# Optimization experiments

Measured on AMD Instinct MI355X. Metric: run time of the kernel, lower is better.

## Reference

```python
import jax, jax.numpy as jnp
import numpy as np

NEG_SLOPE = 0.01  # F.leaky_relu default


def setup_inputs() -> dict:
    key = jax.random.key(0)
    k1, k2, k3, k4 = jax.random.split(key, 4)
    N, F, E = 50000, 64, 800000
    h = jax.random.normal(k1, (N, F), dtype=jnp.float32)
    # attn_fc: Linear(2F, 1, bias=False) -> weight vector of length 2F
    attn_w = jax.random.normal(k2, (2 * F,), dtype=jnp.float32) * (1.0 / np.sqrt(2 * F))
    src = jax.random.randint(k3, (E,), 0, N, dtype=jnp.int32)
    dst = jnp.sort(jax.random.randint(k4, (E,), 0, N, dtype=jnp.int32))
    return {"h": h, "attn_w": attn_w, "src": src, "dst": dst}


def reference(h, attn_w, src, dst):
    N, F = h.shape
    # gather per-edge src/dst features
    z_src = h[src]                      # [E, F]
    z_dst = h[dst]                      # [E, F]
    # cat([z_src, z_dst]) @ w  ==  z_src @ w[:F] + z_dst @ w[F:]
    e = z_src @ attn_w[:F] + z_dst @ attn_w[F:]          # [E]
    e = jnp.where(e >= 0, e, NEG_SLOPE * e)               # leaky_relu
    # segment softmax over incoming edges of each dst node (numerically stable)
    e_max = jax.ops.segment_max(e, dst, num_segments=N)   # [N], -inf for empty
    e_exp = jnp.exp(e - e_max[dst])                       # [E]
    denom = jax.ops.segment_sum(e_exp, dst, num_segments=N)  # [N]
    alpha = e_exp / denom[dst]                            # [E]
    # weighted scatter-sum of src features into dst nodes
    out = jax.ops.segment_sum(alpha[:, None] * z_src, dst, num_segments=N)  # [N, F]
    return out
```

## Files before the change

### kernel.cpp

```cpp
#include <hip/hip_runtime.h>
#include <math.h>

#define NEG_SLOPE 0.01f

__device__ __forceinline__ unsigned short f2bf_rne(float f) {
    unsigned int u = __float_as_uint(f);
    u += 0x7fffu + ((u >> 16) & 1u);
    return (unsigned short)(u >> 16);
}
__device__ __forceinline__ float bf2f(unsigned short b) {
    return __uint_as_float((unsigned int)b << 16);
}

__global__ void prep(const float* __restrict__ h, const float* __restrict__ w,
                     float* __restrict__ a_src, float* __restrict__ a_dst,
                     ushort4* __restrict__ hb, int N) {
    int gid  = blockIdx.x * blockDim.x + threadIdx.x;
    int node = gid >> 4, q = gid & 15;
    if (node >= N) return;
    float4 hv = *(const float4*)(h + (long)node * 64 + q * 4);
    float4 ws = *(const float4*)(w + q * 4);
    float4 wd = *(const float4*)(w + 64 + q * 4);
    ushort4 hb4 = { f2bf_rne(hv.x), f2bf_rne(hv.y), f2bf_rne(hv.z), f2bf_rne(hv.w) };
    hb[(long)node * 16 + q] = hb4;
    float ps = hv.x * ws.x + hv.y * ws.y + hv.z * ws.z + hv.w * ws.w;
    float pd = hv.x * wd.x + hv.y * wd.y + hv.z * wd.z + hv.w * wd.w;
    #pragma unroll
    for (int o = 8; o; o >>= 1) { ps += __shfl_xor(ps, o); pd += __shfl_xor(pd, o); }
    if (q == 0) { a_src[node] = ps; a_dst[node] = pd; }
}

__global__ void edge_e(const int* __restrict__ src, const int* __restrict__ dst,
                       const float* __restrict__ a_src, const float* __restrict__ a_dst,
                       float* __restrict__ e, int* __restrict__ seg, int N, int E) {
    int i0 = (blockIdx.x * blockDim.x + threadIdx.x) * 4;
    if (i0 >= E) return;
    if (i0 + 4 <= E) {
        int4 s4 = *(const int4*)(src + i0);
        int4 d4 = *(const int4*)(dst + i0);
        int prev = (i0 == 0) ? -1 : dst[i0 - 1];
        float4 ev; float t;
        t = a_src[s4.x] + a_dst[d4.x]; ev.x = (t >= 0.f) ? t : NEG_SLOPE * t;
        t = a_src[s4.y] + a_dst[d4.y]; ev.y = (t >= 0.f) ? t : NEG_SLOPE * t;
        t = a_src[s4.z] + a_dst[d4.z]; ev.z = (t >= 0.f) ? t : NEG_SLOPE * t;
        t = a_src[s4.w] + a_dst[d4.w]; ev.w = (t >= 0.f) ? t : NEG_SLOPE * t;
        *(float4*)(e + i0) = ev;
        for (int n = prev + 1; n <= d4.x; ++n) seg[n] = i0;
        for (int n = d4.x + 1; n <= d4.y; ++n) seg[n] = i0 + 1;
        for (int n = d4.y + 1; n <= d4.z; ++n) seg[n] = i0 + 2;
        for (int n = d4.z + 1; n <= d4.w; ++n) seg[n] = i0 + 3;
        if (i0 + 4 == E) { for (int n = d4.w + 1; n <= N; ++n) seg[n] = E; }
    } else {
        for (int i = i0; i < E; ++i) {
            int sj = src[i], dj = dst[i];
            int prev = (i == 0) ? -1 : dst[i - 1];
            float t = a_src[sj] + a_dst[dj];
            e[i] = (t >= 0.f) ? t : NEG_SLOPE * t;
            for (int n = prev + 1; n <= dj; ++n) seg[n] = i;
            if (i == E - 1) { for (int n = dj + 1; n <= N; ++n) seg[n] = E; }
        }
    }
}

__global__ void gat_out(const ushort4* __restrict__ hb, const float* __restrict__ e,
                        const int* __restrict__ src, const int* __restrict__ seg,
                        float* __restrict__ out, int N) {
    int gid  = blockIdx.x * blockDim.x + threadIdx.x;
    int node = gid >> 4;
    if (node >= N) return;
    int tid  = threadIdx.x;
    int lane = tid & 63, q = lane & 15, g = (lane >> 4) & 3, wv = tid >> 6;
    int s    = seg[node];
    int eend = seg[node + 1];
    int deg  = eend - s;
    float* orow = out + (long)node * 64 + q * 4;

    __shared__ float2 pair[4][4][66];

    int wdeg = deg;
    wdeg = max(wdeg, __shfl_xor(wdeg, 16));
    wdeg = max(wdeg, __shfl_xor(wdeg, 32));

    const ushort4* hq = hb + q;
    float4 acc = {0.0f, 0.0f, 0.0f, 0.0f};

    if (wdeg <= 64) {
        float e0 = -INFINITY, e1 = -INFINITY, e2 = -INFINITY, e3 = -INFINITY;
        int   sj0 = 0, sj1 = 0, sj2 = 0, sj3 = 0;
        if (q < deg)      { e0 = e[s + q];      sj0 = src[s + q]; }
        if (q + 16 < deg) { e1 = e[s + q + 16]; sj1 = src[s + q + 16]; }
        if (q + 32 < deg) { e2 = e[s + q + 32]; sj2 = src[s + q + 32]; }
        if (q + 48 < deg) { e3 = e[s + q + 48]; sj3 = src[s + q + 48]; }
        float m = fmaxf(fmaxf(e0, e1), fmaxf(e2, e3));
        #pragma unroll
        for (int o = 8; o; o >>= 1) m = fmaxf(m, __shfl_xor(m, o));
        float p0 = (q < deg)      ? __expf(e0 - m) : 0.0f;
        float p1 = (q + 16 < deg) ? __expf(e1 - m) : 0.0f;
        float p2 = (q + 32 < deg) ? __expf(e2 - m) : 0.0f;
        float p3 = (q + 48 < deg) ? __expf(e3 - m) : 0.0f;
        float dsum = p0 + p1 + p2 + p3;
        #pragma unroll
        for (int o = 8; o; o >>= 1) dsum += __shfl_xor(dsum, o);
        float inv = (dsum > 0.0f) ? (1.0f / dsum) : 0.0f;

        float2* gp = pair[wv][g];
        gp[q]      = make_float2(p0 * inv, __int_as_float(sj0));
        gp[q + 16] = make_float2(p1 * inv, __int_as_float(sj1));
        gp[q + 32] = make_float2(p2 * inv, __int_as_float(sj2));
        gp[q + 48] = make_float2(p3 * inv, __int_as_float(sj3));

        int dr = (deg + 7) & ~7;
        for (int j0 = 0; j0 < dr; j0 += 8) {
            float a_[8]; int s_[8];
            #pragma unroll
            for (int k = 0; k < 8; ++k) {
                float2 pr = gp[j0 + k];
                a_[k] = pr.x; s_[k] = __float_as_int(pr.y);
            }
            ushort4 r_[8];
            #pragma unroll
            for (int k = 0; k < 8; ++k) r_[k] = hq[(long)s_[k] * 16];
            #pragma unroll
            for (int k = 0; k < 8; ++k) {
                acc.x = fmaf(a_[k], bf2f(r_[k].x), acc.x);
                acc.y = fmaf(a_[k], bf2f(r_[k].y), acc.y);
                acc.z = fmaf(a_[k], bf2f(r_[k].z), acc.z);
                acc.w = fmaf(a_[k], bf2f(r_[k].w), acc.w);
            }
        }
        *(float4*)orow = acc;
    } else {
        float m = -INFINITY;
        for (int i = s + q; i < eend; i += 16) m = fmaxf(m, e[i]);
        #pragma unroll
        for (int o = 8; o; o >>= 1) m = fmaxf(m, __shfl_xor(m, o));
        float dsum = 0.0f;
        for (int i = s + q; i < eend; i += 16) dsum += __expf(e[i] - m);
        #pragma unroll
        for (int o = 8; o; o >>= 1) dsum += __shfl_xor(dsum, o);
        float inv = (dsum > 0.0f) ? (1.0f / dsum) : 0.0f;
        for (int i = s; i < eend; ++i) {
            float aj = __expf(e[i] - m) * inv;
            int   sj = src[i];
            ushort4 hv = hq[(long)sj * 16];
            acc.x = fmaf(aj, bf2f(hv.x), acc.x);
            acc.y = fmaf(aj, bf2f(hv.y), acc.y);
            acc.z = fmaf(aj, bf2f(hv.z), acc.z);
            acc.w = fmaf(aj, bf2f(hv.w), acc.w);
        }
        *(float4*)orow = acc;
    }
}

extern "C" void kernel_launch(void* const* d_in, const int* in_sizes, int n_in,
                              void* d_out, int out_size, void* d_ws, size_t ws_size,
                              hipStream_t stream) {
    const float* h   = (const float*)d_in[0];
    const float* w   = (const float*)d_in[1];
    const int*   src = (const int*)d_in[2];
    const int*   dst = (const int*)d_in[3];
    float*       out = (float*)d_out;

    const int F = in_sizes[1] / 2;
    const int N = in_sizes[0] / F;
    const int E = in_sizes[2];

    char*  wsb   = (char*)d_ws;
    float* a_src = (float*)wsb;
    float* a_dst = a_src + N;
    int*   seg   = (int*)(a_dst + N);
    float* ebuf  = (float*)(seg + N + 1);
    size_t off   = (((size_t)(3 * N + 1) + E) * 4 + 255) & ~(size_t)255;
    ushort4* hb  = (ushort4*)(wsb + off);

    prep   <<<dim3((N * 16 + 255) / 256), dim3(256), 0, stream>>>(h, w, a_src, a_dst, hb, N);
    edge_e <<<dim3((E / 4 + 255) / 256), dim3(256), 0, stream>>>(src, dst, a_src, a_dst, ebuf, seg, N, E);
    gat_out<<<dim3((N * 16 + 255) / 256), dim3(256), 0, stream>>>(hb, ebuf, src, seg, out, N);
}
```

Before: 35.74 us.

## Split aggregation into two feature-half passes with separate bf16 tables

The bf16 feature table is split into two 32-column halves stored in separate arrays, and aggregation runs as two kernels, each gathering only 64 bytes per source row. The first pass computes softmax weights and writes normalized alpha back into the edge buffer so the second pass reuses them. The goal is a smaller working set per pass (3.2MB per half) so random gathers hit in cache more often. The cost is an extra launch, re-reading src/e/seg, and per-lane 4-byte gathers instead of 8-byte ones.

```diff
diff --git a/kernel.cpp b/kernel.cpp
--- a/kernel.cpp
+++ b/kernel.cpp
@@ -8,13 +8,12 @@
     u += 0x7fffu + ((u >> 16) & 1u);
     return (unsigned short)(u >> 16);
 }
-__device__ __forceinline__ float bf2f(unsigned short b) {
-    return __uint_as_float((unsigned int)b << 16);
-}
+__device__ __forceinline__ float bf2f_lo(unsigned int u) { return __uint_as_float(u << 16); }
+__device__ __forceinline__ float bf2f_hi(unsigned int u) { return __uint_as_float(u & 0xffff0000u); }
 
 __global__ void prep(const float* __restrict__ h, const float* __restrict__ w,
                      float* __restrict__ a_src, float* __restrict__ a_dst,
-                     ushort4* __restrict__ hb, int N) {
+                     ushort4* __restrict__ hb_lo, ushort4* __restrict__ hb_hi, int N) {
     int gid  = blockIdx.x * blockDim.x + threadIdx.x;
     int node = gid >> 4, q = gid & 15;
     if (node >= N) return;
@@ -22,7 +21,8 @@
     float4 ws = *(const float4*)(w + q * 4);
     float4 wd = *(const float4*)(w + 64 + q * 4);
     ushort4 hb4 = { f2bf_rne(hv.x), f2bf_rne(hv.y), f2bf_rne(hv.z), f2bf_rne(hv.w) };
-    hb[(long)node * 16 + q] = hb4;
+    if (q < 8) hb_lo[(long)node * 8 + q]       = hb4;
+    else       hb_hi[(long)node * 8 + (q - 8)] = hb4;
     float ps = hv.x * ws.x + hv.y * ws.y + hv.z * ws.z + hv.w * ws.w;
     float pd = hv.x * wd.x + hv.y * wd.y + hv.z * wd.z + hv.w * wd.w;
     #pragma unroll
@@ -62,9 +62,9 @@
     }
 }
 
-__global__ void gat_out(const ushort4* __restrict__ hb, const float* __restrict__ e,
-                        const int* __restrict__ src, const int* __restrict__ seg,
-                        float* __restrict__ out, int N) {
+__global__ void gat_lo(const ushort4* __restrict__ hb_lo, float* __restrict__ e,
+                       const int* __restrict__ src, const int* __restrict__ seg,
+                       float* __restrict__ out, int N) {
     int gid  = blockIdx.x * blockDim.x + threadIdx.x;
     int node = gid >> 4;
     if (node >= N) return;
@@ -73,16 +73,15 @@
     int s    = seg[node];
     int eend = seg[node + 1];
     int deg  = eend - s;
-    float* orow = out + (long)node * 64 + q * 4;
-
     __shared__ float2 pair[4][4][66];
+    float2* gp = pair[wv][g];
+    const unsigned int* hq = (const unsigned int*)hb_lo + q;
+    float2 acc = {0.0f, 0.0f};
+    float* orow = out + (long)node * 64 + q * 2;
 
     int wdeg = deg;
     wdeg = max(wdeg, __shfl_xor(wdeg, 16));
     wdeg = max(wdeg, __shfl_xor(wdeg, 32));
-
-    const ushort4* hq = hb + q;
-    float4 acc = {0.0f, 0.0f, 0.0f, 0.0f};
 
     if (wdeg <= 64) {
         float e0 = -INFINITY, e1 = -INFINITY, e2 = -INFINITY, e3 = -INFINITY;
@@ -102,33 +101,36 @@
         #pragma unroll
         for (int o = 8; o; o >>= 1) dsum += __shfl_xor(dsum, o);
         float inv = (dsum > 0.0f) ? (1.0f / dsum) : 0.0f;
-
-        float2* gp = pair[wv][g];
-        gp[q]      = make_float2(p0 * inv, __int_as_float(sj0));
-        gp[q + 16] = make_float2(p1 * inv, __int_as_float(sj1));
-        gp[q + 32] = make_float2(p2 * inv, __int_as_float(sj2));
-        gp[q + 48] = make_float2(p3 * inv, __int_as_float(sj3));
+        p0 *= inv; p1 *= inv; p2 *= inv; p3 *= inv;
+
+        if (q < deg)      e[s + q]      = p0;
+        if (q + 16 < deg) e[s + q + 16] = p1;
+        if (q + 32 < deg) e[s + q + 32] = p2;
+        if (q + 48 < deg) e[s + q + 48] = p3;
+
+        gp[q]      = make_float2(p0, __int_as_float(sj0));
+        gp[q + 16] = make_float2(p1, __int_as_float(sj1));
+        gp[q + 32] = make_float2(p2, __int_as_float(sj2));
+        gp[q + 48] = make_float2(p3, __int_as_float(sj3));
 
         int dr = (deg + 7) & ~7;
         for (int j0 = 0; j0 < dr; j0 += 8) {
             float a_[8]; int s_[8];
             #pragma unroll
             for (int k = 0; k < 8; ++k) {
-                float2 pr = gp[j0 + k];
-                a_[k] = pr.x; s_[k] = __float_as_int(pr.y);
-            }
-            ushort4 r_[8];
+                float2 pv = gp[j0 + k];
+                a_[k] = pv.x; s_[k] = __float_as_int(pv.y);
+            }
+            unsigned int r_[8];
             #pragma unroll
             for (int k = 0; k < 8; ++k) r_[k] = hq[(long)s_[k] * 16];
             #pragma unroll
             for (int k = 0; k < 8; ++k) {
-                acc.x = fmaf(a_[k], bf2f(r_[k].x), acc.x);
-                acc.y = fmaf(a_[k], bf2f(r_[k].y), acc.y);
-                acc.z = fmaf(a_[k], bf2f(r_[k].z), acc.z);
-                acc.w = fmaf(a_[k], bf2f(r_[k].w), acc.w);
-            }
-        }
-        *(float4*)orow = acc;
+                acc.x = fmaf(a_[k], bf2f_lo(r_[k]), acc.x);
+                acc.y = fmaf(a_[k], bf2f_hi(r_[k]), acc.y);
+            }
+        }
+        *(float2*)orow = acc;
     } else {
         float m = -INFINITY;
         for (int i = s + q; i < eend; i += 16) m = fmaxf(m, e[i]);
@@ -142,13 +144,76 @@
         for (int i = s; i < eend; ++i) {
             float aj = __expf(e[i] - m) * inv;
             int   sj = src[i];
-            ushort4 hv = hq[(long)sj * 16];
-            acc.x = fmaf(aj, bf2f(hv.x), acc.x);
-            acc.y = fmaf(aj, bf2f(hv.y), acc.y);
-            acc.z = fmaf(aj, bf2f(hv.z), acc.z);
-            acc.w = fmaf(aj, bf2f(hv.w), acc.w);
-        }
-        *(float4*)orow = acc;
+            unsigned int u = hq[(long)sj * 16];
+            acc.x = fmaf(aj, bf2f_lo(u), acc.x);
+            acc.y = fmaf(aj, bf2f_hi(u), acc.y);
+        }
+        *(float2*)orow = acc;
+        for (int i = s + q; i < eend; i += 16)
+            e[i] = __expf(e[i] - m) * inv;
+    }
+}
+
+__global__ void gat_hi(const ushort4* __restrict__ hb_hi, const float* __restrict__ e,
+                       const int* __restrict__ src, const int* __restrict__ seg,
+                       float* __restrict__ out, int N) {
+    int gid  = blockIdx.x * blockDim.x + threadIdx.x;
+    int node = gid >> 4;
+    if (node >= N) return;
+    int tid  = threadIdx.x;
+    int lane = tid & 63, q = lane & 15, g = (lane >> 4) & 3, wv = tid >> 6;
+    int s    = seg[node];
+    int eend = seg[node + 1];
+    int deg  = eend - s;
+    __shared__ float2 pair[4][4][66];
+    float2* gp = pair[wv][g];
+    const unsigned int* hq = (const unsigned int*)hb_hi + q;
+    float2 acc = {0.0f, 0.0f};
+    float* orow = out + (long)node * 64 + 32 + q * 2;
+
+    int wdeg = deg;
+    wdeg = max(wdeg, __shfl_xor(wdeg, 16));
+    wdeg = max(wdeg, __shfl_xor(wdeg, 32));
+
+    if (wdeg <= 64) {
+        float p0 = 0.f, p1 = 0.f, p2 = 0.f, p3 = 0.f;
+        int   sj0 = 0, sj1 = 0, sj2 = 0, sj3 = 0;
+        if (q < deg)      { p0 = e[s + q];      sj0 = src[s + q]; }
+        if (q + 16 < deg) { p1 = e[s + q + 16]; sj1 = src[s + q + 16]; }
+        if (q + 32 < deg) { p2 = e[s + q + 32]; sj2 = src[s + q + 32]; }
+        if (q + 48 < deg) { p3 = e[s + q + 48]; sj3 = src[s + q + 48]; }
+        gp[q]      = make_float2(p0, __int_as_float(sj0));
+        gp[q + 16] = make_float2(p1, __int_as_float(sj1));
+        gp[q + 32] = make_float2(p2, __int_as_float(sj2));
+        gp[q + 48] = make_float2(p3, __int_as_float(sj3));
+
+        int dr = (deg + 7) & ~7;
+        for (int j0 = 0; j0 < dr; j0 += 8) {
+            float a_[8]; int s_[8];
+            #pragma unroll
+            for (int k = 0; k < 8; ++k) {
+                float2 pv = gp[j0 + k];
+                a_[k] = pv.x; s_[k] = __float_as_int(pv.y);
+            }
+            unsigned int r_[8];
+            #pragma unroll
+            for (int k = 0; k < 8; ++k) r_[k] = hq[(long)s_[k] * 16];
+            #pragma unroll
+            for (int k = 0; k < 8; ++k) {
+                acc.x = fmaf(a_[k], bf2f_lo(r_[k]), acc.x);
+                acc.y = fmaf(a_[k], bf2f_hi(r_[k]), acc.y);
+            }
+        }
+        *(float2*)orow = acc;
+    } else {
+        for (int i = s; i < eend; ++i) {
+            float aj = e[i];
+            int   sj = src[i];
+            unsigned int u = hq[(long)sj * 16];
+            acc.x = fmaf(aj, bf2f_lo(u), acc.x);
+            acc.y = fmaf(aj, bf2f_hi(u), acc.y);
+        }
+        *(float2*)orow = acc;
     }
 }
 
@@ -165,15 +230,17 @@
     const int N = in_sizes[0] / F;
     const int E = in_sizes[2];
 
-    char*  wsb   = (char*)d_ws;
-    float* a_src = (float*)wsb;
-    float* a_dst = a_src + N;
-    int*   seg   = (int*)(a_dst + N);
-    float* ebuf  = (float*)(seg + N + 1);
-    size_t off   = (((size_t)(3 * N + 1) + E) * 4 + 255) & ~(size_t)255;
-    ushort4* hb  = (ushort4*)(wsb + off);
-
-    prep   <<<dim3((N * 16 + 255) / 256), dim3(256), 0, stream>>>(h, w, a_src, a_dst, hb, N);
+    char*    wsb   = (char*)d_ws;
+    float*   a_src = (float*)wsb;
+    float*   a_dst = a_src + N;
+    int*     seg   = (int*)(a_dst + N);
+    float*   ebuf  = (float*)(seg + N + 1);
+    size_t   off   = (((size_t)(3 * N + 1) + E) * 4 + 255) & ~(size_t)255;
+    ushort4* hb_lo = (ushort4*)(wsb + off);
+    ushort4* hb_hi = hb_lo + (long)N * 8;
+
+    prep   <<<dim3((N * 16 + 255) / 256), dim3(256), 0, stream>>>(h, w, a_src, a_dst, hb_lo, hb_hi, N);
     edge_e <<<dim3((E / 4 + 255) / 256), dim3(256), 0, stream>>>(src, dst, a_src, a_dst, ebuf, seg, N, E);
-    gat_out<<<dim3((N * 16 + 255) / 256), dim3(256), 0, stream>>>(hb, ebuf, src, seg, out, N);
-}
+    gat_lo <<<dim3((N * 16 + 255) / 256), dim3(256), 0, stream>>>(hb_lo, ebuf, src, seg, out, N);
+    gat_hi <<<dim3((N * 16 + 255) / 256), dim3(256), 0, stream>>>(hb_hi, ebuf, src, seg, out, N);
+}
```

Result: slower. 40.52 us (+13.4%).

## Fuse prep and segment build into one launch, recompute edge scores in aggregation

Applied to the files above, without the earlier changes.

Merges the node-projection/bf16-conversion kernel and the segment-offset construction into a single launch, using disjoint block ranges. The per-edge score buffer is dropped: the aggregation kernel now recomputes leaky_relu(a_src[src]+a_dst[node]) on the fly. This removes one kernel launch and the E-sized write and read of scores, at the cost of extra gathers of a_src inside aggregation. Nontemporal load/store hints are also added for h and the output.

```diff
diff --git a/kernel.cpp b/kernel.cpp
--- a/kernel.cpp
+++ b/kernel.cpp
@@ -2,6 +2,8 @@
 #include <math.h>
 
 #define NEG_SLOPE 0.01f
+
+typedef float f32x4 __attribute__((ext_vector_type(4)));
 
 __device__ __forceinline__ unsigned short f2bf_rne(float f) {
     unsigned int u = __float_as_uint(f);
@@ -12,59 +14,50 @@
     return __uint_as_float((unsigned int)b << 16);
 }
 
-__global__ void prep(const float* __restrict__ h, const float* __restrict__ w,
-                     float* __restrict__ a_src, float* __restrict__ a_dst,
-                     ushort4* __restrict__ hb, int N) {
-    int gid  = blockIdx.x * blockDim.x + threadIdx.x;
-    int node = gid >> 4, q = gid & 15;
-    if (node >= N) return;
-    float4 hv = *(const float4*)(h + (long)node * 64 + q * 4);
-    float4 ws = *(const float4*)(w + q * 4);
-    float4 wd = *(const float4*)(w + 64 + q * 4);
-    ushort4 hb4 = { f2bf_rne(hv.x), f2bf_rne(hv.y), f2bf_rne(hv.z), f2bf_rne(hv.w) };
-    hb[(long)node * 16 + q] = hb4;
-    float ps = hv.x * ws.x + hv.y * ws.y + hv.z * ws.z + hv.w * ws.w;
-    float pd = hv.x * wd.x + hv.y * wd.y + hv.z * wd.z + hv.w * wd.w;
-    #pragma unroll
-    for (int o = 8; o; o >>= 1) { ps += __shfl_xor(ps, o); pd += __shfl_xor(pd, o); }
-    if (q == 0) { a_src[node] = ps; a_dst[node] = pd; }
-}
-
-__global__ void edge_e(const int* __restrict__ src, const int* __restrict__ dst,
-                       const float* __restrict__ a_src, const float* __restrict__ a_dst,
-                       float* __restrict__ e, int* __restrict__ seg, int N, int E) {
-    int i0 = (blockIdx.x * blockDim.x + threadIdx.x) * 4;
-    if (i0 >= E) return;
-    if (i0 + 4 <= E) {
-        int4 s4 = *(const int4*)(src + i0);
-        int4 d4 = *(const int4*)(dst + i0);
-        int prev = (i0 == 0) ? -1 : dst[i0 - 1];
-        float4 ev; float t;
-        t = a_src[s4.x] + a_dst[d4.x]; ev.x = (t >= 0.f) ? t : NEG_SLOPE * t;
-        t = a_src[s4.y] + a_dst[d4.y]; ev.y = (t >= 0.f) ? t : NEG_SLOPE * t;
-        t = a_src[s4.z] + a_dst[d4.z]; ev.z = (t >= 0.f) ? t : NEG_SLOPE * t;
-        t = a_src[s4.w] + a_dst[d4.w]; ev.w = (t >= 0.f) ? t : NEG_SLOPE * t;
-        *(float4*)(e + i0) = ev;
-        for (int n = prev + 1; n <= d4.x; ++n) seg[n] = i0;
-        for (int n = d4.x + 1; n <= d4.y; ++n) seg[n] = i0 + 1;
-        for (int n = d4.y + 1; n <= d4.z; ++n) seg[n] = i0 + 2;
-        for (int n = d4.z + 1; n <= d4.w; ++n) seg[n] = i0 + 3;
-        if (i0 + 4 == E) { for (int n = d4.w + 1; n <= N; ++n) seg[n] = E; }
+__global__ void prep2(const float* __restrict__ h, const float* __restrict__ w,
+                      const int* __restrict__ dst,
+                      float* __restrict__ a_src, float* __restrict__ a_dst,
+                      int* __restrict__ seg, ushort4* __restrict__ hb,
+                      int N, int E, int PB) {
+    if ((int)blockIdx.x < PB) {
+        int gid  = blockIdx.x * blockDim.x + threadIdx.x;
+        int node = gid >> 4, q = gid & 15;
+        if (node >= N) return;
+        f32x4 hv = __builtin_nontemporal_load((const f32x4*)(h + (long)node * 64 + q * 4));
+        float4 ws = *(const float4*)(w + q * 4);
+        float4 wd = *(const float4*)(w + 64 + q * 4);
+        ushort4 hb4 = { f2bf_rne(hv.x), f2bf_rne(hv.y), f2bf_rne(hv.z), f2bf_rne(hv.w) };
+        hb[(long)node * 16 + q] = hb4;
+        float ps = hv.x * ws.x + hv.y * ws.y + hv.z * ws.z + hv.w * ws.w;
+        float pd = hv.x * wd.x + hv.y * wd.y + hv.z * wd.z + hv.w * wd.w;
+        #pragma unroll
+        for (int o = 8; o; o >>= 1) { ps += __shfl_xor(ps, o); pd += __shfl_xor(pd, o); }
+        if (q == 0) { a_src[node] = ps; a_dst[node] = pd; }
     } else {
-        for (int i = i0; i < E; ++i) {
-            int sj = src[i], dj = dst[i];
-            int prev = (i == 0) ? -1 : dst[i - 1];
-            float t = a_src[sj] + a_dst[dj];
-            e[i] = (t >= 0.f) ? t : NEG_SLOPE * t;
-            for (int n = prev + 1; n <= dj; ++n) seg[n] = i;
-            if (i == E - 1) { for (int n = dj + 1; n <= N; ++n) seg[n] = E; }
+        int i0 = ((blockIdx.x - PB) * blockDim.x + threadIdx.x) * 4;
+        if (i0 >= E) return;
+        if (i0 + 4 <= E) {
+            int4 d4 = *(const int4*)(dst + i0);
+            int prev = (i0 == 0) ? -1 : dst[i0 - 1];
+            for (int n = prev + 1; n <= d4.x; ++n) seg[n] = i0;
+            for (int n = d4.x + 1; n <= d4.y; ++n) seg[n] = i0 + 1;
+            for (int n = d4.y + 1; n <= d4.z; ++n) seg[n] = i0 + 2;
+            for (int n = d4.z + 1; n <= d4.w; ++n) seg[n] = i0 + 3;
+            if (i0 + 4 == E) { for (int n = d4.w + 1; n <= N; ++n) seg[n] = E; }
+        } else {
+            for (int i = i0; i < E; ++i) {
+                int dj = dst[i];
+                int prev = (i == 0) ? -1 : dst[i - 1];
+                for (int n = prev + 1; n <= dj; ++n) seg[n] = i;
+                if (i == E - 1) { for (int n = dj + 1; n <= N; ++n) seg[n] = E; }
+            }
         }
     }
 }
 
-__global__ void gat_out(const ushort4* __restrict__ hb, const float* __restrict__ e,
-                        const int* __restrict__ src, const int* __restrict__ seg,
-                        float* __restrict__ out, int N) {
+__global__ void gat_out(const ushort4* __restrict__ hb, const float* __restrict__ a_src,
+                        const float* __restrict__ a_dst, const int* __restrict__ src,
+                        const int* __restrict__ seg, float* __restrict__ out, int N) {
     int gid  = blockIdx.x * blockDim.x + threadIdx.x;
     int node = gid >> 4;
     if (node >= N) return;
@@ -73,24 +66,25 @@
     int s    = seg[node];
     int eend = seg[node + 1];
     int deg  = eend - s;
+    __shared__ float2 pair[4][4][66];
+    float2* gp = pair[wv][g];
+    const ushort4* hq = hb + q;
+    float4 acc = {0.0f, 0.0f, 0.0f, 0.0f};
     float* orow = out + (long)node * 64 + q * 4;
-
-    __shared__ float2 pair[4][4][66];
 
     int wdeg = deg;
     wdeg = max(wdeg, __shfl_xor(wdeg, 16));
     wdeg = max(wdeg, __shfl_xor(wdeg, 32));
 
-    const ushort4* hq = hb + q;
-    float4 acc = {0.0f, 0.0f, 0.0f, 0.0f};
+    float ad = a_dst[node];
 
     if (wdeg <= 64) {
         float e0 = -INFINITY, e1 = -INFINITY, e2 = -INFINITY, e3 = -INFINITY;
         int   sj0 = 0, sj1 = 0, sj2 = 0, sj3 = 0;
-        if (q < deg)      { e0 = e[s + q];      sj0 = src[s + q]; }
-        if (q + 16 < deg) { e1 = e[s + q + 16]; sj1 = src[s + q + 16]; }
-        if (q + 32 < deg) { e2 = e[s + q + 32]; sj2 = src[s + q + 32]; }
-        if (q + 48 < deg) { e3 = e[s + q + 48]; sj3 = src[s + q + 48]; }
+        if (q < deg)      { sj0 = src[s + q];      float t = a_src[sj0] + ad; e0 = (t >= 0.f) ? t : NEG_SLOPE * t; }
+        if (q + 16 < deg) { sj1 = src[s + q + 16]; float t = a_src[sj1] + ad; e1 = (t >= 0.f) ? t : NEG_SLOPE * t; }
+        if (q + 32 < deg) { sj2 = src[s + q + 32]; float t = a_src[sj2] + ad; e2 = (t >= 0.f) ? t : NEG_SLOPE * t; }
+        if (q + 48 < deg) { sj3 = src[s + q + 48]; float t = a_src[sj3] + ad; e3 = (t >= 0.f) ? t : NEG_SLOPE * t; }
         float m = fmaxf(fmaxf(e0, e1), fmaxf(e2, e3));
         #pragma unroll
         for (int o = 8; o; o >>= 1) m = fmaxf(m, __shfl_xor(m, o));
@@ -103,7 +97,6 @@
         for (int o = 8; o; o >>= 1) dsum += __shfl_xor(dsum, o);
         float inv = (dsum > 0.0f) ? (1.0f / dsum) : 0.0f;
 
-        float2* gp = pair[wv][g];
         gp[q]      = make_float2(p0 * inv, __int_as_float(sj0));
         gp[q + 16] = make_float2(p1 * inv, __int_as_float(sj1));
         gp[q + 32] = make_float2(p2 * inv, __int_as_float(sj2));
@@ -114,8 +107,8 @@
             float a_[8]; int s_[8];
             #pragma unroll
             for (int k = 0; k < 8; ++k) {
-                float2 pr = gp[j0 + k];
-                a_[k] = pr.x; s_[k] = __float_as_int(pr.y);
+                float2 pv = gp[j0 + k];
+                a_[k] = pv.x; s_[k] = __float_as_int(pv.y);
             }
             ushort4 r_[8];
             #pragma unroll
@@ -128,27 +121,39 @@
                 acc.w = fmaf(a_[k], bf2f(r_[k].w), acc.w);
             }
         }
-        *(float4*)orow = acc;
+        f32x4 v; v.x = acc.x; v.y = acc.y; v.z = acc.z; v.w = acc.w;
+        __builtin_nontemporal_store(v, (f32x4*)orow);
     } else {
         float m = -INFINITY;
-        for (int i = s + q; i < eend; i += 16) m = fmaxf(m, e[i]);
+        for (int i = s + q; i < eend; i += 16) {
+            float t = a_src[src[i]] + ad;
+            t = (t >= 0.f) ? t : NEG_SLOPE * t;
+            m = fmaxf(m, t);
+        }
         #pragma unroll
         for (int o = 8; o; o >>= 1) m = fmaxf(m, __shfl_xor(m, o));
         float dsum = 0.0f;
-        for (int i = s + q; i < eend; i += 16) dsum += __expf(e[i] - m);
+        for (int i = s + q; i < eend; i += 16) {
+            float t = a_src[src[i]] + ad;
+            t = (t >= 0.f) ? t : NEG_SLOPE * t;
+            dsum += __expf(t - m);
+        }
         #pragma unroll
         for (int o = 8; o; o >>= 1) dsum += __shfl_xor(dsum, o);
         float inv = (dsum > 0.0f) ? (1.0f / dsum) : 0.0f;
         for (int i = s; i < eend; ++i) {
-            float aj = __expf(e[i] - m) * inv;
             int   sj = src[i];
+            float t  = a_src[sj] + ad;
+            t = (t >= 0.f) ? t : NEG_SLOPE * t;
+            float aj = __expf(t - m) * inv;
             ushort4 hv = hq[(long)sj * 16];
             acc.x = fmaf(aj, bf2f(hv.x), acc.x);
             acc.y = fmaf(aj, bf2f(hv.y), acc.y);
             acc.z = fmaf(aj, bf2f(hv.z), acc.z);
             acc.w = fmaf(aj, bf2f(hv.w), acc.w);
         }
-        *(float4*)orow = acc;
+        f32x4 v; v.x = acc.x; v.y = acc.y; v.z = acc.z; v.w = acc.w;
+        __builtin_nontemporal_store(v, (f32x4*)orow);
     }
 }
 
@@ -165,15 +170,15 @@
     const int N = in_sizes[0] / F;
     const int E = in_sizes[2];
 
-    char*  wsb   = (char*)d_ws;
-    float* a_src = (float*)wsb;
-    float* a_dst = a_src + N;
-    int*   seg   = (int*)(a_dst + N);
-    float* ebuf  = (float*)(seg + N + 1);
-    size_t off   = (((size_t)(3 * N + 1) + E) * 4 + 255) & ~(size_t)255;
-    ushort4* hb  = (ushort4*)(wsb + off);
+    char*    wsb   = (char*)d_ws;
+    float*   a_src = (float*)wsb;
+    float*   a_dst = a_src + N;
+    int*     seg   = (int*)(a_dst + N);
+    size_t   off   = ((size_t)(3 * N + 1) * 4 + 255) & ~(size_t)255;
+    ushort4* hb    = (ushort4*)(wsb + off);
 
-    prep   <<<dim3((N * 16 + 255) / 256), dim3(256), 0, stream>>>(h, w, a_src, a_dst, hb, N);
-    edge_e <<<dim3((E / 4 + 255) / 256), dim3(256), 0, stream>>>(src, dst, a_src, a_dst, ebuf, seg, N, E);
-    gat_out<<<dim3((N * 16 + 255) / 256), dim3(256), 0, stream>>>(hb, ebuf, src, seg, out, N);
+    const int PB = (N * 16 + 255) / 256;
+    const int SB = ((E + 3) / 4 + 255) / 256;
+    prep2  <<<dim3(PB + SB), dim3(256), 0, stream>>>(h, w, dst, a_src, a_dst, seg, hb, N, E, PB);
+    gat_out<<<dim3((N * 16 + 255) / 256), dim3(256), 0, stream>>>(hb, a_src, a_dst, src, seg, out, N);
 }
```

Measured after the change: 33.18 us. 1.08x faster.
